# Optimization experiments

Hardware: AMD Instinct MI355X
Metric: run time of the kernel (lower is better)

The kernel has to match this reference:

```python
import jax, jax.numpy as jnp
import numpy as np

TOPK = 20
EPS = 1e-5
NEG_SLOPE = 0.2


def _bn(x, gamma, beta):
    # BatchNorm1d in training mode: stats over all but the channel (last) axis.
    axes = tuple(range(x.ndim - 1))
    m = x.mean(axes, keepdims=True)
    v = x.var(axes, keepdims=True)  # biased variance, as torch uses for normalization
    return (x - m) * jax.lax.rsqrt(v + EPS) * gamma + beta


def setup_inputs() -> dict:
    key = jax.random.key(0)
    ks = jax.random.split(key, 12)
    B, N, F, D, K = 64, 512, 64, 64, TOPK
    H = 32  # slide_win // 2
    return {
        "data": jax.random.normal(ks[0], (B, N, F), jnp.float32),
        "org_edge_index": jax.random.randint(ks[1], (2, 10), 0, N),  # unused by forward math
        "emb_table": jax.random.normal(ks[2], (N, D), jnp.float32) * 0.1,
        "W_gnn": jax.random.normal(ks[3], (D, F), jnp.float32) / jnp.sqrt(F),
        "att_i": jax.random.normal(ks[4], (D,), jnp.float32) / jnp.sqrt(D),
        "att_j": jax.random.normal(ks[5], (D,), jnp.float32) / jnp.sqrt(D),
        "att_em_i": jax.random.normal(ks[6], (D,), jnp.float32) / jnp.sqrt(D),
        "att_em_j": jax.random.normal(ks[7], (D,), jnp.float32) / jnp.sqrt(D),
        "bias_gnn": jnp.zeros((D,), jnp.float32),
        "bn1_g": jnp.ones((D,), jnp.float32), "bn1_b": jnp.zeros((D,), jnp.float32),
        "bn2_g": jnp.ones((D,), jnp.float32), "bn2_b": jnp.zeros((D,), jnp.float32),
        "lin_W": jax.random.normal(ks[8], (H, D), jnp.float32) / jnp.sqrt(D),
        "lin_b": jnp.zeros((H,), jnp.float32),
        "out_W": jax.random.normal(ks[9], (2 * H, H), jnp.float32) / jnp.sqrt(H),
        "out_b": jnp.zeros((2 * H,), jnp.float32),
    }


def reference(data, org_edge_index, emb_table, W_gnn, att_i, att_j, att_em_i, att_em_j,
              bias_gnn, bn1_g, bn1_b, bn2_g, bn2_b, lin_W, lin_b, out_W, out_b):
    B, N, F = data.shape
    # --- top-k cosine-similarity graph (embeddings are detached in the original) ---
    w = emb_table  # (N, D)
    nrm = jnp.linalg.norm(w, axis=-1)
    cos = (w @ w.T) / (nrm[:, None] * nrm[None, :])
    _, topk_idx = jax.lax.top_k(cos, TOPK)  # (N, K); col 0 is the self loop (cos=1)
    # Every target node i has exactly TOPK incoming edges j in topk_idx[i];
    # remove_self_loops + add_self_loops is set-equivalent to this edge set.

    # --- GraphLayer (GAT-style, heads=1, concat=False) ---
    xw = jnp.einsum('bnf,df->bnd', data, W_gnn)  # (B, N, D)
    a_i = xw @ att_i + w @ att_em_i              # (B, N), per-target scalar
    a_j = xw @ att_j + w @ att_em_j              # (B, N), per-source scalar
    alpha = a_i[:, :, None] + a_j[:, topk_idx]   # (B, N, K): gather sources per target
    alpha = jax.nn.leaky_relu(alpha, NEG_SLOPE)
    alpha = jax.nn.softmax(alpha, axis=-1)       # segment softmax over fixed-size neighborhoods
    xj = xw[:, topk_idx]                         # (B, N, K, D) edge gather (memory-bound)
    out = jnp.einsum('bnk,bnkd->bnd', alpha, xj) + bias_gnn  # scatter-aggregate

    # GNNLayer: BatchNorm1d over (B*N) rows + ReLU
    out = jax.nn.relu(_bn(out, bn1_g, bn1_b))

    # --- head ---
    out = out * w                                 # x * embedding(idx)
    out = jax.nn.relu(_bn(out, bn2_g, bn2_b))     # bn_outlayer_in over (B, D, N)
    out = out @ lin_W.T + lin_b                   # (B, N, slide_win//2)
    out = out @ out_W.T + out_b                   # OutLayer, single Linear -> (B, N, slide_win)
    return out
```

## Files before the change

kernel.cpp:

```cpp
#include <hip/hip_runtime.h>
#include <math.h>

#define Bb 64
#define Nn 512
#define Ff 64
#define Dd 64
#define Kk 20
#define Hh 32
#define ROWS (Bb*Nn)
#define EPSc 1e-5f
#define NEG 0.2f


__device__ __forceinline__ float dot4(float4 a, float4 b) {
    return a.x*b.x + a.y*b.y + a.z*b.z + a.w*b.w;
}

__global__ __launch_bounds__(256) void k_topk(const float* __restrict__ emb,
                                              int* __restrict__ topk,
                                              float* __restrict__ stats) {
    __shared__ __align__(16) float wish[64];
    __shared__ float sv[512];
    int i = blockIdx.x, t = threadIdx.x;
    if (i == 0) stats[t] = (t < 256) ? 0.f : stats[t];
    if (t < 64) {
        float wv = emb[i*64 + t];
        float ss = wv*wv;
        #pragma unroll
        for (int s = 32; s > 0; s >>= 1) ss += __shfl_xor(ss, s);
        wish[t] = wv * (1.f / sqrtf(ss));
    }
    __syncthreads();
    int seg = t & 3;
    int jl  = t >> 2;
    const float4* wish4 = (const float4*)wish;
    float4 wn[4];
    #pragma unroll
    for (int q = 0; q < 4; q++) wn[q] = wish4[seg*4 + q];
    const float4* emb4 = (const float4*)emb;
    for (int jb = 0; jb < 8; jb++) {
        int j = jb*64 + jl;
        float p = 0.f, s2 = 0.f;
        #pragma unroll
        for (int q = 0; q < 4; q++) {
            float4 e = emb4[j*16 + seg*4 + q];
            p  += dot4(e, wn[q]);
            s2 += dot4(e, e);
        }
        p  += __shfl_xor(p, 1);  p  += __shfl_xor(p, 2);
        s2 += __shfl_xor(s2, 1); s2 += __shfl_xor(s2, 2);
        if (seg == 0) sv[j] = p * (1.f / sqrtf(s2));
    }
    __syncthreads();
    if (t < 64) {
        float v[8];
        #pragma unroll
        for (int q = 0; q < 8; q++) v[q] = sv[q*64 + t];
        for (int k = 0; k < Kk; k++) {
            float bv = v[0]; int bi = t;
            #pragma unroll
            for (int q = 1; q < 8; q++)
                if (v[q] > bv) { bv = v[q]; bi = q*64 + t; }
            #pragma unroll
            for (int s = 1; s < 64; s <<= 1) {
                float ov = __shfl_xor(bv, s); int oi = __shfl_xor(bi, s);
                if (ov > bv || (ov == bv && oi < bi)) { bv = ov; bi = oi; }
            }
            if (t == 0) topk[i*Kk + k] = bi;
            #pragma unroll
            for (int q = 0; q < 8; q++)
                if (bi == q*64 + t) v[q] = -INFINITY;
        }
    }
}

__global__ __launch_bounds__(256) void k_xw(const float* __restrict__ data,
                                            const float* __restrict__ emb,
                                            const float* __restrict__ Wg,
                                            const float* __restrict__ att_i,
                                            const float* __restrict__ att_j,
                                            const float* __restrict__ att_em_i,
                                            const float* __restrict__ att_em_j,
                                            float* __restrict__ xw,
                                            float* __restrict__ ai,
                                            float* __restrict__ aj) {
    __shared__ __align__(16) float sh[256];
    int t = threadIdx.x;
    int d = t & 63, r = t >> 6;
    const float4* wg4 = (const float4*)Wg;
    float4 w4[16];
    #pragma unroll
    for (int q = 0; q < 16; q++) w4[q] = wg4[d*16 + q];
    float atti = att_i[d], attj = att_j[d];
    float aemi = att_em_i[d], aemj = att_em_j[d];
    const float4* sh4 = (const float4*)sh;
    for (int g = blockIdx.x; g < ROWS/4; g += 1024) {
        sh[t] = data[g*256 + t];
        __syncthreads();
        float acc = 0.f;
        #pragma unroll
        for (int q = 0; q < 16; q++) acc += dot4(sh4[r*16 + q], w4[q]);
        int row = g*4 + r;
        xw[row*64 + d] = acc;
        int n = row & (Nn - 1);
        float wv = emb[n*64 + d];
        float vi = acc*atti + wv*aemi;
        float vj = acc*attj + wv*aemj;
        #pragma unroll
        for (int s = 32; s > 0; s >>= 1) { vi += __shfl_xor(vi, s); vj += __shfl_xor(vj, s); }
        if (d == 0) { ai[row] = vi; aj[row] = vj; }
        __syncthreads();
    }
}

__global__ __launch_bounds__(256) void k_gnn(const float* __restrict__ xw,
                                             const float* __restrict__ ai,
                                             const float* __restrict__ aj,
                                             const int* __restrict__ topk,
                                             const float* __restrict__ bias,
                                             float* __restrict__ gout,
                                             float* __restrict__ stats) {
    int t = threadIdx.x;
    int d = t & 63, r = t >> 6;
    int xcd = blockIdx.x & 7, sub = blockIdx.x >> 3;
    float bias_d = bias[d];
    float lsum = 0.f, lsq = 0.f;
    for (int it = 0; it < 8; it++) {
        int g = xcd*1024 + it*128 + sub;
        int row = g*4 + r;
        int b = row >> 9;
        int n = row & (Nn - 1);
        float aival = ai[row];
        float e[Kk]; int idxs[Kk];
        float m = -INFINITY;
        #pragma unroll
        for (int k = 0; k < Kk; k++) {
            int j = topk[n*Kk + k];
            idxs[k] = j;
            float v = aival + aj[(b << 9) + j];
            v = v > 0.f ? v : NEG * v;
            e[k] = v; m = fmaxf(m, v);
        }
        float s = 0.f;
        #pragma unroll
        for (int k = 0; k < Kk; k++) { e[k] = __expf(e[k] - m); s += e[k]; }
        float invs = 1.f / s;
        float acc = bias_d;
        #pragma unroll
        for (int k = 0; k < Kk; k++)
            acc += e[k] * invs * xw[((b << 9) + idxs[k])*64 + d];
        gout[row*64 + d] = acc;
        lsum += acc; lsq += acc*acc;
    }
    __shared__ float ssum[4][64], ssq[4][64];
    ssum[r][d] = lsum; ssq[r][d] = lsq;
    __syncthreads();
    if (t < 64) {
        float s1 = ssum[0][t] + ssum[1][t] + ssum[2][t] + ssum[3][t];
        float s2 = ssq[0][t] + ssq[1][t] + ssq[2][t] + ssq[3][t];
        atomicAdd(&stats[t], s1);
        atomicAdd(&stats[64 + t], s2);
    }
}

__global__ void k_bnfin(float* stats, const float* __restrict__ g,
                        const float* __restrict__ bta, int which) {
    int d = threadIdx.x;
    float mean = stats[which*128 + d]      * (1.f / ROWS);
    float ex2  = stats[which*128 + 64 + d] * (1.f / ROWS);
    float var  = ex2 - mean*mean;
    float istd = 1.f / sqrtf(var + EPSc);
    float A = istd * g[d];
    stats[256 + which*128 + d]      = A;
    stats[256 + which*128 + 64 + d] = bta[d] - mean * A;
}

__global__ __launch_bounds__(256) void k_bn1mul(float* __restrict__ gout,
                                                const float* __restrict__ emb,
                                                float* __restrict__ stats) {
    int t = threadIdx.x;
    int d = t & 63, r = t >> 6;
    const float A = stats[256 + d], C = stats[320 + d];
    float lsum = 0.f, lsq = 0.f;
    for (int row0 = blockIdx.x*4; row0 < ROWS; row0 += gridDim.x*4) {
        int row = row0 + r;
        int n = row & (Nn - 1);
        float x = gout[row*64 + d];
        float v = x*A + C;
        v = v > 0.f ? v : 0.f;
        v *= emb[n*64 + d];
        gout[row*64 + d] = v;
        lsum += v; lsq += v*v;
    }
    __shared__ float ssum[4][64], ssq[4][64];
    ssum[r][d] = lsum; ssq[r][d] = lsq;
    __syncthreads();
    if (t < 64) {
        float s1 = ssum[0][t] + ssum[1][t] + ssum[2][t] + ssum[3][t];
        float s2 = ssq[0][t] + ssq[1][t] + ssq[2][t] + ssq[3][t];
        atomicAdd(&stats[128 + t], s1);
        atomicAdd(&stats[192 + t], s2);
    }
}

__global__ __launch_bounds__(256) void k_head(const float* __restrict__ y,
                                              const float* __restrict__ stats,
                                              const float* __restrict__ linW,
                                              const float* __restrict__ linb,
                                              const float* __restrict__ outW,
                                              const float* __restrict__ outb,
                                              float* __restrict__ out) {
    __shared__ __align__(16) float zsh[4][64];
    __shared__ __align__(16) float hsh[4][32];
    int t = threadIdx.x;
    int d = t & 63, r = t >> 6;
    int j = d & 31, half = d >> 5;
    float A = stats[384 + d], C = stats[448 + d];
    const float4* linW4 = (const float4*)linW;
    const float4* outW4 = (const float4*)outW;
    float4 lw4[8], ow4[8];
    #pragma unroll
    for (int q = 0; q < 8; q++) lw4[q] = linW4[j*16 + half*8 + q];
    #pragma unroll
    for (int q = 0; q < 8; q++) ow4[q] = outW4[d*8 + q];
    float lb = linb[j], ob = outb[d];
    const float4* zsh4 = (const float4*)zsh;
    const float4* hsh4 = (const float4*)hsh;
    for (int g = blockIdx.x; g < ROWS/4; g += 512) {
        int row = g*4 + r;
        float x = y[row*64 + d];
        float z = fmaxf(x*A + C, 0.f);
        zsh[r][d] = z;
        __syncthreads();
        float p = 0.f;
        #pragma unroll
        for (int q = 0; q < 8; q++) p += dot4(zsh4[r*16 + half*8 + q], lw4[q]);
        p += __shfl_xor(p, 32);
        float h = p + lb;
        if (half == 0) hsh[r][j] = h;
        __syncthreads();
        float o = ob;
        #pragma unroll
        for (int q = 0; q < 8; q++) o += dot4(hsh4[r*8 + q], ow4[q]);
        out[row*64 + d] = o;
        __syncthreads();
    }
}

extern "C" void kernel_launch(void* const* d_in, const int* in_sizes, int n_in,
                              void* d_out, int out_size, void* d_ws, size_t ws_size,
                              hipStream_t stream) {
    const float* data     = (const float*)d_in[0];
    const float* emb      = (const float*)d_in[2];
    const float* Wg       = (const float*)d_in[3];
    const float* att_i    = (const float*)d_in[4];
    const float* att_j    = (const float*)d_in[5];
    const float* att_em_i = (const float*)d_in[6];
    const float* att_em_j = (const float*)d_in[7];
    const float* bias     = (const float*)d_in[8];
    const float* bn1_g    = (const float*)d_in[9];
    const float* bn1_b    = (const float*)d_in[10];
    const float* bn2_g    = (const float*)d_in[11];
    const float* bn2_b    = (const float*)d_in[12];
    const float* linW     = (const float*)d_in[13];
    const float* linb     = (const float*)d_in[14];
    const float* outW     = (const float*)d_in[15];
    const float* outb     = (const float*)d_in[16];
    float* out = (float*)d_out;

    float* ws       = (float*)d_ws;
    int*   topk     = (int*)(ws + 512);
    float* stats    = ws + 10752;
    float* a_i      = ws + 11264;
    float* a_j      = ws + 44032;
    float* xw       = ws + 76800;
    float* gout     = ws + 2173952;

    k_topk  <<<Nn, 256, 0, stream>>>(emb, topk, stats);
    k_xw    <<<1024, 256, 0, stream>>>(data, emb, Wg, att_i, att_j, att_em_i, att_em_j,
                                       xw, a_i, a_j);
    k_gnn   <<<1024, 256, 0, stream>>>(xw, a_i, a_j, topk, bias, gout, stats);
    k_bnfin <<<1, 64, 0, stream>>>(stats, bn1_g, bn1_b, 0);
    k_bn1mul<<<1024, 256, 0, stream>>>(gout, emb, stats);
    k_bnfin <<<1, 64, 0, stream>>>(stats, bn2_g, bn2_b, 1);
    k_head  <<<512, 256, 0, stream>>>(gout, stats, linW, linb, outW, outb, out);
}
```

Before: 222.4 us.

## Merge topk with projection kernel, fold BN finalize, vectorize GNN gather

The top-k similarity blocks and the data projection blocks now run in one launch, with the block index choosing the role. The two single-block BN finalize kernels are removed; each consumer recomputes the BN scale and shift from the accumulated stats. The GNN aggregation puts the 20 neighbors across lanes, does the softmax with wave shuffles, and gathers xw as float4. The BN1 pass is vectorized to float4, and the head kernel uses an XCD-aware row mapping. The aim is to cut launch count, let the serial top-k overlap the projection, and raise memory efficiency of the gather. The cost is more shuffle work and duplicated per-block BN finalize arithmetic.

New measurement: 349.4 us. 57.1% more time.

```diff
diff --git a/kernel.cpp b/kernel.cpp
--- a/kernel.cpp
+++ b/kernel.cpp
@@ -15,207 +15,260 @@
 __device__ __forceinline__ float dot4(float4 a, float4 b) {
     return a.x*b.x + a.y*b.y + a.z*b.z + a.w*b.w;
 }
-
-__global__ __launch_bounds__(256) void k_topk(const float* __restrict__ emb,
-                                              int* __restrict__ topk,
-                                              float* __restrict__ stats) {
-    __shared__ __align__(16) float wish[64];
-    __shared__ float sv[512];
-    int i = blockIdx.x, t = threadIdx.x;
-    if (i == 0) stats[t] = (t < 256) ? 0.f : stats[t];
-    if (t < 64) {
-        float wv = emb[i*64 + t];
-        float ss = wv*wv;
-        #pragma unroll
-        for (int s = 32; s > 0; s >>= 1) ss += __shfl_xor(ss, s);
-        wish[t] = wv * (1.f / sqrtf(ss));
-    }
-    __syncthreads();
-    int seg = t & 3;
-    int jl  = t >> 2;
-    const float4* wish4 = (const float4*)wish;
-    float4 wn[4];
-    #pragma unroll
-    for (int q = 0; q < 4; q++) wn[q] = wish4[seg*4 + q];
-    const float4* emb4 = (const float4*)emb;
-    for (int jb = 0; jb < 8; jb++) {
-        int j = jb*64 + jl;
-        float p = 0.f, s2 = 0.f;
-        #pragma unroll
-        for (int q = 0; q < 4; q++) {
-            float4 e = emb4[j*16 + seg*4 + q];
-            p  += dot4(e, wn[q]);
-            s2 += dot4(e, e);
-        }
-        p  += __shfl_xor(p, 1);  p  += __shfl_xor(p, 2);
-        s2 += __shfl_xor(s2, 1); s2 += __shfl_xor(s2, 2);
-        if (seg == 0) sv[j] = p * (1.f / sqrtf(s2));
-    }
-    __syncthreads();
-    if (t < 64) {
-        float v[8];
-        #pragma unroll
-        for (int q = 0; q < 8; q++) v[q] = sv[q*64 + t];
-        for (int k = 0; k < Kk; k++) {
-            float bv = v[0]; int bi = t;
-            #pragma unroll
-            for (int q = 1; q < 8; q++)
-                if (v[q] > bv) { bv = v[q]; bi = q*64 + t; }
-            #pragma unroll
-            for (int s = 1; s < 64; s <<= 1) {
-                float ov = __shfl_xor(bv, s); int oi = __shfl_xor(bi, s);
-                if (ov > bv || (ov == bv && oi < bi)) { bv = ov; bi = oi; }
-            }
-            if (t == 0) topk[i*Kk + k] = bi;
-            #pragma unroll
-            for (int q = 0; q < 8; q++)
-                if (bi == q*64 + t) v[q] = -INFINITY;
-        }
-    }
-}
-
-__global__ __launch_bounds__(256) void k_xw(const float* __restrict__ data,
+__device__ __forceinline__ void xr4(float4& a, int m) {
+    a.x += __shfl_xor(a.x, m); a.y += __shfl_xor(a.y, m);
+    a.z += __shfl_xor(a.z, m); a.w += __shfl_xor(a.w, m);
+}
+
+__global__ __launch_bounds__(256) void k_p1(const float* __restrict__ data,
                                             const float* __restrict__ emb,
                                             const float* __restrict__ Wg,
                                             const float* __restrict__ att_i,
                                             const float* __restrict__ att_j,
                                             const float* __restrict__ att_em_i,
                                             const float* __restrict__ att_em_j,
-                                            float* __restrict__ xw,
+                                            int* __restrict__ topk,
+                                            float* __restrict__ stats,
                                             float* __restrict__ ai,
-                                            float* __restrict__ aj) {
-    __shared__ __align__(16) float sh[256];
+                                            float* __restrict__ aj,
+                                            float* __restrict__ xw) {
+    __shared__ __align__(16) float shbuf[576];
+    int t = threadIdx.x, blk = blockIdx.x;
+    if (blk < Nn) {
+        float* wish = shbuf;
+        float* sv   = shbuf + 64;
+        int i = blk;
+        if (t < 64) {
+            float wv = emb[i*64 + t];
+            float ss = wv*wv;
+            #pragma unroll
+            for (int s = 32; s > 0; s >>= 1) ss += __shfl_xor(ss, s);
+            wish[t] = wv * (1.f / sqrtf(ss));
+        }
+        __syncthreads();
+        int seg = t & 3, jl = t >> 2;
+        const float4* wish4 = (const float4*)wish;
+        float4 wn[4];
+        #pragma unroll
+        for (int q = 0; q < 4; q++) wn[q] = wish4[seg*4 + q];
+        const float4* emb4 = (const float4*)emb;
+        for (int jb = 0; jb < 8; jb++) {
+            int j = jb*64 + jl;
+            float p = 0.f, s2 = 0.f;
+            #pragma unroll
+            for (int q = 0; q < 4; q++) {
+                float4 e = emb4[j*16 + seg*4 + q];
+                p += dot4(e, wn[q]); s2 += dot4(e, e);
+            }
+            p  += __shfl_xor(p, 1);  p  += __shfl_xor(p, 2);
+            s2 += __shfl_xor(s2, 1); s2 += __shfl_xor(s2, 2);
+            if (seg == 0) sv[j] = p * (1.f / sqrtf(s2));
+        }
+        __syncthreads();
+        if (t < 64) {
+            float v[8];
+            #pragma unroll
+            for (int q = 0; q < 8; q++) v[q] = sv[q*64 + t];
+            for (int k = 0; k < Kk; k++) {
+                float bv = v[0]; int bi = t;
+                #pragma unroll
+                for (int q = 1; q < 8; q++)
+                    if (v[q] > bv) { bv = v[q]; bi = q*64 + t; }
+                #pragma unroll
+                for (int s = 1; s < 64; s <<= 1) {
+                    float ov = __shfl_xor(bv, s); int oi = __shfl_xor(bi, s);
+                    if (ov > bv || (ov == bv && oi < bi)) { bv = ov; bi = oi; }
+                }
+                if (t == 0) topk[i*Kk + k] = bi;
+                #pragma unroll
+                for (int q = 0; q < 8; q++)
+                    if (bi == q*64 + t) v[q] = -INFINITY;
+            }
+        }
+    } else {
+        if (blk == Nn) stats[t] = 0.f;
+        float* sh = shbuf;
+        int xcd = blk & 7, sub2 = (blk - Nn) >> 3;
+        int d = t & 63, r = t >> 6;
+        const float4* wg4 = (const float4*)Wg;
+        float4 w4[16];
+        #pragma unroll
+        for (int q = 0; q < 16; q++) w4[q] = wg4[d*16 + q];
+        float atti = att_i[d], attj = att_j[d];
+        float aemi = att_em_i[d], aemj = att_em_j[d];
+        const float4* sh4 = (const float4*)sh;
+        for (int it = 0; it < 16; it++) {
+            int g = xcd*1024 + it*64 + sub2;
+            sh[t] = data[g*256 + t];
+            __syncthreads();
+            float acc = 0.f;
+            #pragma unroll
+            for (int q = 0; q < 16; q++) acc += dot4(sh4[r*16 + q], w4[q]);
+            int row = g*4 + r;
+            xw[row*64 + d] = acc;
+            int n = row & (Nn - 1);
+            float wv = emb[n*64 + d];
+            float vi = acc*atti + wv*aemi;
+            float vj = acc*attj + wv*aemj;
+            #pragma unroll
+            for (int s = 32; s > 0; s >>= 1) { vi += __shfl_xor(vi, s); vj += __shfl_xor(vj, s); }
+            if (d == 0) { ai[row] = vi; aj[row] = vj; }
+            __syncthreads();
+        }
+    }
+}
+
+__global__ __launch_bounds__(256) void k_gnn2(const float* __restrict__ xw,
+                                              const float* __restrict__ ai,
+                                              const float* __restrict__ aj,
+                                              const int* __restrict__ topk,
+                                              const float* __restrict__ bias,
+                                              float* __restrict__ gout,
+                                              float* __restrict__ stats) {
+    __shared__ __align__(16) float4 s1[4][16], s2[4][16];
     int t = threadIdx.x;
-    int d = t & 63, r = t >> 6;
-    const float4* wg4 = (const float4*)Wg;
-    float4 w4[16];
-    #pragma unroll
-    for (int q = 0; q < 16; q++) w4[q] = wg4[d*16 + q];
-    float atti = att_i[d], attj = att_j[d];
-    float aemi = att_em_i[d], aemj = att_em_j[d];
-    const float4* sh4 = (const float4*)sh;
-    for (int g = blockIdx.x; g < ROWS/4; g += 1024) {
-        sh[t] = data[g*256 + t];
-        __syncthreads();
-        float acc = 0.f;
-        #pragma unroll
-        for (int q = 0; q < 16; q++) acc += dot4(sh4[r*16 + q], w4[q]);
-        int row = g*4 + r;
-        xw[row*64 + d] = acc;
-        int n = row & (Nn - 1);
-        float wv = emb[n*64 + d];
-        float vi = acc*atti + wv*aemi;
-        float vj = acc*attj + wv*aemj;
-        #pragma unroll
-        for (int s = 32; s > 0; s >>= 1) { vi += __shfl_xor(vi, s); vj += __shfl_xor(vj, s); }
-        if (d == 0) { ai[row] = vi; aj[row] = vj; }
-        __syncthreads();
-    }
-}
-
-__global__ __launch_bounds__(256) void k_gnn(const float* __restrict__ xw,
-                                             const float* __restrict__ ai,
-                                             const float* __restrict__ aj,
-                                             const int* __restrict__ topk,
-                                             const float* __restrict__ bias,
-                                             float* __restrict__ gout,
-                                             float* __restrict__ stats) {
-    int t = threadIdx.x;
-    int d = t & 63, r = t >> 6;
     int xcd = blockIdx.x & 7, sub = blockIdx.x >> 3;
-    float bias_d = bias[d];
-    float lsum = 0.f, lsq = 0.f;
+    int l = t & 63, w = t >> 6;
+    int q = l & 15, kg = l >> 4, kk = l & 31;
+    const float4* xw4 = (const float4*)xw;
+    float4* gout4 = (float4*)gout;
+    float4 bias4 = ((const float4*)bias)[q];
+    float4 sum4 = {0,0,0,0}, sq4 = {0,0,0,0};
     for (int it = 0; it < 8; it++) {
         int g = xcd*1024 + it*128 + sub;
-        int row = g*4 + r;
-        int b = row >> 9;
-        int n = row & (Nn - 1);
+        int row = g*4 + w;
+        int b = row >> 9, n = row & (Nn - 1);
+        int base = b << 9;
         float aival = ai[row];
-        float e[Kk]; int idxs[Kk];
-        float m = -INFINITY;
-        #pragma unroll
-        for (int k = 0; k < Kk; k++) {
-            int j = topk[n*Kk + k];
-            idxs[k] = j;
-            float v = aival + aj[(b << 9) + j];
-            v = v > 0.f ? v : NEG * v;
-            e[k] = v; m = fmaxf(m, v);
-        }
-        float s = 0.f;
-        #pragma unroll
-        for (int k = 0; k < Kk; k++) { e[k] = __expf(e[k] - m); s += e[k]; }
-        float invs = 1.f / s;
-        float acc = bias_d;
-        #pragma unroll
-        for (int k = 0; k < Kk; k++)
-            acc += e[k] * invs * xw[((b << 9) + idxs[k])*64 + d];
-        gout[row*64 + d] = acc;
-        lsum += acc; lsq += acc*acc;
-    }
-    __shared__ float ssum[4][64], ssq[4][64];
-    ssum[r][d] = lsum; ssq[r][d] = lsq;
+        int j = 0; float v = -1e30f;
+        if (kk < Kk) {
+            j = topk[n*Kk + kk];
+            float x = aival + aj[base + j];
+            v = x > 0.f ? x : NEG * x;
+        }
+        float m = v;
+        #pragma unroll
+        for (int s = 1; s <= 16; s <<= 1) m = fmaxf(m, __shfl_xor(m, s));
+        float e = (kk < Kk) ? __expf(v - m) : 0.f;
+        float es = e;
+        #pragma unroll
+        for (int s = 1; s <= 16; s <<= 1) es += __shfl_xor(es, s);
+        float alpha = e * (1.f / es);
+        float4 acc = {0,0,0,0};
+        #pragma unroll
+        for (int i = 0; i < 5; i++) {
+            int k = i*4 + kg;
+            float ak = __shfl(alpha, k);
+            int   jk = __shfl(j, k);
+            float4 xv = xw4[(base + jk)*16 + q];
+            acc.x += ak*xv.x; acc.y += ak*xv.y; acc.z += ak*xv.z; acc.w += ak*xv.w;
+        }
+        xr4(acc, 16); xr4(acc, 32);
+        if (l < 16) {
+            float4 r4;
+            r4.x = acc.x + bias4.x; r4.y = acc.y + bias4.y;
+            r4.z = acc.z + bias4.z; r4.w = acc.w + bias4.w;
+            gout4[row*16 + q] = r4;
+            sum4.x += r4.x; sum4.y += r4.y; sum4.z += r4.z; sum4.w += r4.w;
+            sq4.x += r4.x*r4.x; sq4.y += r4.y*r4.y; sq4.z += r4.z*r4.z; sq4.w += r4.w*r4.w;
+        }
+    }
+    if (l < 16) { s1[w][q] = sum4; s2[w][q] = sq4; }
     __syncthreads();
-    if (t < 64) {
-        float s1 = ssum[0][t] + ssum[1][t] + ssum[2][t] + ssum[3][t];
-        float s2 = ssq[0][t] + ssq[1][t] + ssq[2][t] + ssq[3][t];
-        atomicAdd(&stats[t], s1);
-        atomicAdd(&stats[64 + t], s2);
-    }
-}
-
-__global__ void k_bnfin(float* stats, const float* __restrict__ g,
-                        const float* __restrict__ bta, int which) {
-    int d = threadIdx.x;
-    float mean = stats[which*128 + d]      * (1.f / ROWS);
-    float ex2  = stats[which*128 + 64 + d] * (1.f / ROWS);
-    float var  = ex2 - mean*mean;
-    float istd = 1.f / sqrtf(var + EPSc);
-    float A = istd * g[d];
-    stats[256 + which*128 + d]      = A;
-    stats[256 + which*128 + 64 + d] = bta[d] - mean * A;
-}
-
-__global__ __launch_bounds__(256) void k_bn1mul(float* __restrict__ gout,
-                                                const float* __restrict__ emb,
-                                                float* __restrict__ stats) {
+    if (t < 16) {
+        float4 a = s1[0][t], c = s2[0][t];
+        #pragma unroll
+        for (int ww = 1; ww < 4; ww++) {
+            float4 x1 = s1[ww][t], x2 = s2[ww][t];
+            a.x += x1.x; a.y += x1.y; a.z += x1.z; a.w += x1.w;
+            c.x += x2.x; c.y += x2.y; c.z += x2.z; c.w += x2.w;
+        }
+        atomicAdd(&stats[4*t+0], a.x); atomicAdd(&stats[4*t+1], a.y);
+        atomicAdd(&stats[4*t+2], a.z); atomicAdd(&stats[4*t+3], a.w);
+        atomicAdd(&stats[64+4*t+0], c.x); atomicAdd(&stats[64+4*t+1], c.y);
+        atomicAdd(&stats[64+4*t+2], c.z); atomicAdd(&stats[64+4*t+3], c.w);
+    }
+}
+
+__global__ __launch_bounds__(256) void k_bn1(float* __restrict__ gout,
+                                             const float* __restrict__ emb,
+                                             const float* __restrict__ bn1_g,
+                                             const float* __restrict__ bn1_b,
+                                             float* __restrict__ stats) {
+    __shared__ __align__(16) float4 s1[4][16], s2[4][16];
     int t = threadIdx.x;
-    int d = t & 63, r = t >> 6;
-    const float A = stats[256 + d], C = stats[320 + d];
-    float lsum = 0.f, lsq = 0.f;
-    for (int row0 = blockIdx.x*4; row0 < ROWS; row0 += gridDim.x*4) {
-        int row = row0 + r;
-        int n = row & (Nn - 1);
-        float x = gout[row*64 + d];
-        float v = x*A + C;
-        v = v > 0.f ? v : 0.f;
-        v *= emb[n*64 + d];
-        gout[row*64 + d] = v;
-        lsum += v; lsq += v*v;
-    }
-    __shared__ float ssum[4][64], ssq[4][64];
-    ssum[r][d] = lsum; ssq[r][d] = lsq;
+    int xcd = blockIdx.x & 7, sub = blockIdx.x >> 3;
+    int q = t & 15;
+    float4 A4, C4;
+    {
+        float* Ap = &A4.x; float* Cp = &C4.x;
+        #pragma unroll
+        for (int c = 0; c < 4; c++) {
+            int d = 4*q + c;
+            float mean = stats[d] * (1.f/ROWS);
+            float ex2  = stats[64+d] * (1.f/ROWS);
+            float var  = ex2 - mean*mean;
+            float A = (1.f / sqrtf(var + EPSc)) * bn1_g[d];
+            Ap[c] = A; Cp[c] = bn1_b[d] - mean * A;
+        }
+    }
+    float4* gout4 = (float4*)gout;
+    const float4* emb4 = (const float4*)emb;
+    float4 sum4 = {0,0,0,0}, sq4 = {0,0,0,0};
+    #pragma unroll
+    for (int i = 0; i < 2; i++) {
+        int f = xcd*65536 + i*32768 + sub*256 + t;
+        int row = f >> 4, n = row & (Nn - 1);
+        float4 x = gout4[f];
+        float4 wv = emb4[n*16 + q];
+        float4 v;
+        v.x = fmaxf(x.x*A4.x + C4.x, 0.f) * wv.x;
+        v.y = fmaxf(x.y*A4.y + C4.y, 0.f) * wv.y;
+        v.z = fmaxf(x.z*A4.z + C4.z, 0.f) * wv.z;
+        v.w = fmaxf(x.w*A4.w + C4.w, 0.f) * wv.w;
+        gout4[f] = v;
+        sum4.x += v.x; sum4.y += v.y; sum4.z += v.z; sum4.w += v.w;
+        sq4.x += v.x*v.x; sq4.y += v.y*v.y; sq4.z += v.z*v.z; sq4.w += v.w*v.w;
+    }
+    xr4(sum4, 16); xr4(sum4, 32);
+    xr4(sq4, 16);  xr4(sq4, 32);
+    int l = t & 63, w = t >> 6;
+    if (l < 16) { s1[w][q] = sum4; s2[w][q] = sq4; }
     __syncthreads();
-    if (t < 64) {
-        float s1 = ssum[0][t] + ssum[1][t] + ssum[2][t] + ssum[3][t];
-        float s2 = ssq[0][t] + ssq[1][t] + ssq[2][t] + ssq[3][t];
-        atomicAdd(&stats[128 + t], s1);
-        atomicAdd(&stats[192 + t], s2);
-    }
-}
-
-__global__ __launch_bounds__(256) void k_head(const float* __restrict__ y,
-                                              const float* __restrict__ stats,
-                                              const float* __restrict__ linW,
-                                              const float* __restrict__ linb,
-                                              const float* __restrict__ outW,
-                                              const float* __restrict__ outb,
-                                              float* __restrict__ out) {
+    if (t < 16) {
+        float4 a = s1[0][t], c = s2[0][t];
+        #pragma unroll
+        for (int ww = 1; ww < 4; ww++) {
+            float4 x1 = s1[ww][t], x2 = s2[ww][t];
+            a.x += x1.x; a.y += x1.y; a.z += x1.z; a.w += x1.w;
+            c.x += x2.x; c.y += x2.y; c.z += x2.z; c.w += x2.w;
+        }
+        atomicAdd(&stats[128+4*t+0], a.x); atomicAdd(&stats[128+4*t+1], a.y);
+        atomicAdd(&stats[128+4*t+2], a.z); atomicAdd(&stats[128+4*t+3], a.w);
+        atomicAdd(&stats[192+4*t+0], c.x); atomicAdd(&stats[192+4*t+1], c.y);
+        atomicAdd(&stats[192+4*t+2], c.z); atomicAdd(&stats[192+4*t+3], c.w);
+    }
+}
+
+__global__ __launch_bounds__(256) void k_head2(const float* __restrict__ y,
+                                               const float* __restrict__ stats,
+                                               const float* __restrict__ bn2_g,
+                                               const float* __restrict__ bn2_b,
+                                               const float* __restrict__ linW,
+                                               const float* __restrict__ linb,
+                                               const float* __restrict__ outW,
+                                               const float* __restrict__ outb,
+                                               float* __restrict__ out) {
     __shared__ __align__(16) float zsh[4][64];
     __shared__ __align__(16) float hsh[4][32];
     int t = threadIdx.x;
     int d = t & 63, r = t >> 6;
     int j = d & 31, half = d >> 5;
-    float A = stats[384 + d], C = stats[448 + d];
+    float mean = stats[128+d] * (1.f/ROWS);
+    float ex2  = stats[192+d] * (1.f/ROWS);
+    float var  = ex2 - mean*mean;
+    float A = (1.f / sqrtf(var + EPSc)) * bn2_g[d];
+    float C = bn2_b[d] - mean * A;
     const float4* linW4 = (const float4*)linW;
     const float4* outW4 = (const float4*)outW;
     float4 lw4[8], ow4[8];
@@ -226,7 +279,9 @@
     float lb = linb[j], ob = outb[d];
     const float4* zsh4 = (const float4*)zsh;
     const float4* hsh4 = (const float4*)hsh;
-    for (int g = blockIdx.x; g < ROWS/4; g += 512) {
+    int xcd = blockIdx.x & 7, sub = blockIdx.x >> 3;
+    for (int it = 0; it < 8; it++) {
+        int g = xcd*1024 + it*128 + sub;
         int row = g*4 + r;
         float x = y[row*64 + d];
         float z = fmaxf(x*A + C, 0.f);
@@ -236,8 +291,7 @@
         #pragma unroll
         for (int q = 0; q < 8; q++) p += dot4(zsh4[r*16 + half*8 + q], lw4[q]);
         p += __shfl_xor(p, 32);
-        float h = p + lb;
-        if (half == 0) hsh[r][j] = h;
+        if (half == 0) hsh[r][j] = p + lb;
         __syncthreads();
         float o = ob;
         #pragma unroll
@@ -268,20 +322,18 @@
     const float* outb     = (const float*)d_in[16];
     float* out = (float*)d_out;
 
-    float* ws       = (float*)d_ws;
-    int*   topk     = (int*)(ws + 512);
-    float* stats    = ws + 10752;
-    float* a_i      = ws + 11264;
-    float* a_j      = ws + 44032;
-    float* xw       = ws + 76800;
-    float* gout     = ws + 2173952;
-
-    k_topk  <<<Nn, 256, 0, stream>>>(emb, topk, stats);
-    k_xw    <<<1024, 256, 0, stream>>>(data, emb, Wg, att_i, att_j, att_em_i, att_em_j,
-                                       xw, a_i, a_j);
-    k_gnn   <<<1024, 256, 0, stream>>>(xw, a_i, a_j, topk, bias, gout, stats);
-    k_bnfin <<<1, 64, 0, stream>>>(stats, bn1_g, bn1_b, 0);
-    k_bn1mul<<<1024, 256, 0, stream>>>(gout, emb, stats);
-    k_bnfin <<<1, 64, 0, stream>>>(stats, bn2_g, bn2_b, 1);
-    k_head  <<<512, 256, 0, stream>>>(gout, stats, linW, linb, outW, outb, out);
-}
+    float* ws    = (float*)d_ws;
+    int*   topk  = (int*)(ws + 512);
+    float* stats = ws + 10752;
+    float* a_i   = ws + 11264;
+    float* a_j   = ws + 44032;
+    float* xw    = ws + 76800;
+    float* gout  = ws + 2173952;
+
+    k_p1   <<<1024, 256, 0, stream>>>(data, emb, Wg, att_i, att_j, att_em_i, att_em_j,
+                                      topk, stats, a_i, a_j, xw);
+    k_gnn2 <<<1024, 256, 0, stream>>>(xw, a_i, a_j, topk, bias, gout, stats);
+    k_bn1  <<<1024, 256, 0, stream>>>(gout, emb, bn1_g, bn1_b, stats);
+    k_head2<<<1024, 256, 0, stream>>>(gout, stats, bn2_g, bn2_b,
+                                      linW, linb, outW, outb, out);
+}
```
